# Optimization experiments

Hardware: AMD Instinct MI355X
Metric: run time of the kernel (lower is better)

Reference implementation:

```python
import jax, jax.numpy as jnp
import numpy as np

N = 50000      # nodes
E = 400000     # edges (avg degree 8)
N_IN = 256     # n_in_chan
N_HID = 256    # n_hid_chan


def gcn_conv(x, src, dst, W, b, n):
    """PyG GCNConv: D^{-1/2}(A+I)D^{-1/2} X W^T + b (add_self_loops=True, unit weights)."""
    h = x @ W.T                                           # [n, out]
    # degree over A + I: each node has a self loop (the initial ones) plus in-edges
    deg = jnp.ones((n,), h.dtype).at[dst].add(1.0)        # [n]
    dinv = jax.lax.rsqrt(deg)                             # deg >= 1 always
    norm = dinv[src] * dinv[dst]                          # [E]
    agg = jnp.zeros_like(h).at[dst].add(h[src] * norm[:, None])
    agg = agg + h * (dinv * dinv)[:, None]                # self-loop term, norm = dinv_i^2
    return agg + b


def setup_inputs() -> dict:
    key = jax.random.key(0)
    k1, k2, k3, k4 = jax.random.split(key, 4)
    x = jax.random.normal(k1, (N, N_IN + N_HID), dtype=jnp.float32)
    edge_index = jax.random.randint(k2, (2, E), 0, N, dtype=jnp.int64)
    s1 = 1.0 / np.sqrt(N_IN + N_HID)
    s2 = 1.0 / np.sqrt(N_HID)
    W1 = jax.random.normal(k3, (N_HID, N_IN + N_HID), dtype=jnp.float32) * s1
    W2 = jax.random.normal(k4, (N_HID, N_HID), dtype=jnp.float32) * s2
    b1 = jnp.zeros((N_HID,), jnp.float32)
    b2 = jnp.zeros((N_HID,), jnp.float32)
    return {"x": x, "edge_index": edge_index, "W1": W1, "b1": b1, "W2": W2, "b2": b2}


def reference(x, edge_index, W1, b1, W2, b2):
    src, dst = edge_index[0], edge_index[1]
    h = jax.nn.relu(gcn_conv(x, src, dst, W1, b1, N))
    return gcn_conv(h, src, dst, W2, b2, N)
```

## Files before the change

kernel.cpp:

```cpp
#include <hip/hip_runtime.h>
#include <hip/hip_bf16.h>

#define NN 50000
#define CH 256
#define SLOTS 96
#define G1K 512
#define G2K 256

typedef unsigned short u16;
typedef unsigned int   u32;

using short8 = __attribute__((ext_vector_type(8))) short;
using u16x8  = __attribute__((ext_vector_type(8))) unsigned short;
using f32x4  = __attribute__((ext_vector_type(4))) float;

static __device__ __forceinline__ float4 ld4(const float* p){ return *(const float4*)p; }

static __device__ __forceinline__ u16 f2b(float f){
  u32 u = __float_as_uint(f);
  u = (u + 0x7fffu + ((u >> 16) & 1u)) >> 16;
  return (u16)u;
}
static __device__ __forceinline__ float b2f(u16 b){
  return __uint_as_float(((u32)b) << 16);
}
static __device__ __forceinline__ int pkbf(float lo, float hi){
  __hip_bfloat162 h = __float22bfloat162_rn(make_float2(lo, hi));
  int r; __builtin_memcpy(&r, &h, 4); return r;
}

static __device__ __forceinline__ void gload_lds16(const u16* g, u16* l){
  __builtin_amdgcn_global_load_lds((const __attribute__((address_space(1))) void*)g,
                                   (__attribute__((address_space(3))) void*)l, 16, 0, 0);
}

#define WBAR(vm) do{ \
    asm volatile("s_waitcnt vmcnt(" #vm ") lgkmcnt(0)" ::: "memory"); \
    __builtin_amdgcn_s_barrier(); \
  }while(0)


__global__ void ell_build_kernel(const int* __restrict__ src, const int* __restrict__ dst,
                                 int* __restrict__ deg, int* __restrict__ ell, int E,
                                 const float* __restrict__ X,  u16* __restrict__ Xbf,  int xn4,
                                 const float* __restrict__ W1, u16* __restrict__ W1bf, int w1n4,
                                 const float* __restrict__ W2, u16* __restrict__ W2bf, int w2n4){
  int T = gridDim.x * 256;
  int g = blockIdx.x*256 + threadIdx.x;
  if (g < E){
    int d = dst[g];
    int pos = atomicAdd(&deg[d], 1);
    if (pos < SLOTS) ell[(size_t)d*SLOTS + pos] = src[g];
  }
  for (int i = g; i < xn4; i += T){
    float4 v = ld4(X + (size_t)i*4);
    int2 o = { pkbf(v.x,v.y), pkbf(v.z,v.w) };
    *(int2*)(Xbf + (size_t)i*4) = o;
  }
  for (int i = g; i < w1n4; i += T){
    float4 v = ld4(W1 + (size_t)i*4);
    int2 o = { pkbf(v.x,v.y), pkbf(v.z,v.w) };
    *(int2*)(W1bf + (size_t)i*4) = o;
  }
  for (int i = g; i < w2n4; i += T){
    float4 v = ld4(W2 + (size_t)i*4);
    int2 o = { pkbf(v.x,v.y), pkbf(v.z,v.w) };
    *(int2*)(W2bf + (size_t)i*4) = o;
  }
}


#define G1_GLB(kt, bb) do{ \
    gload_lds16(gA + (size_t)(kt)*32,          &As[bb][wave*512]); \
    gload_lds16(gB + (size_t)(kt)*32,          &Bs[bb][wave*2048]); \
    gload_lds16(gB + (size_t)(kt)*32 + 16*G1K, &Bs[bb][wave*2048 + 512]); \
    gload_lds16(gB + (size_t)(kt)*32 + 32*G1K, &Bs[bb][wave*2048 + 1024]); \
    gload_lds16(gB + (size_t)(kt)*32 + 48*G1K, &Bs[bb][wave*2048 + 1536]); \
  }while(0)

#define G1_COMP(rb) do{ \
    short8 af[4], bq[4]; \
    _Pragma("unroll") \
    for (int i=0;i<4;i++) af[i] = *(const short8*)&As[rb][(i*16 + lm)*32 + lk]; \
    _Pragma("unroll") \
    for (int j=0;j<4;j++) bq[j] = *(const short8*)&Bs[rb][(wave*64 + j*16 + lm)*32 + lk]; \
    _Pragma("unroll") \
    for (int i=0;i<4;i++) \
      _Pragma("unroll") \
      for (int j=0;j<4;j++) \
        acc[i][j] = __builtin_amdgcn_mfma_f32_16x16x32_bf16(af[i], bq[j], acc[i][j], 0, 0, 0); \
  }while(0)

__global__ __launch_bounds__(256, 4) void gemm1_kernel(const u16* __restrict__ A,
                                                       const u16* __restrict__ Bbf,
                                                       u16* __restrict__ C, int M){
  __shared__ u16 As[3][64*32];
  __shared__ u16 Bs[3][256*32];
  int tid = threadIdx.x;
  int wave = tid >> 6, lane = tid & 63;
  int bm = blockIdx.x;

  int ar = bm*64 + wave*16 + (lane>>2); if (ar > M-1) ar = M-1;
  const u16* gA = A + (size_t)ar*G1K + (lane&3)*8;
  const u16* gB = Bbf + (size_t)(wave*64 + (lane>>2))*G1K + (lane&3)*8;

  int lm = lane & 15;
  int lk = (lane >> 4) * 8;

  f32x4 acc[4][4] = {};

  G1_GLB(0, 0);
  G1_GLB(1, 1);
  WBAR(5);

  G1_GLB( 2,2); G1_COMP(0); WBAR(5);
  G1_GLB( 3,0); G1_COMP(1); WBAR(5);
  G1_GLB( 4,1); G1_COMP(2); WBAR(5);
  G1_GLB( 5,2); G1_COMP(0); WBAR(5);
  G1_GLB( 6,0); G1_COMP(1); WBAR(5);
  G1_GLB( 7,1); G1_COMP(2); WBAR(5);
  G1_GLB( 8,2); G1_COMP(0); WBAR(5);
  G1_GLB( 9,0); G1_COMP(1); WBAR(5);
  G1_GLB(10,1); G1_COMP(2); WBAR(5);
  G1_GLB(11,2); G1_COMP(0); WBAR(5);
  G1_GLB(12,0); G1_COMP(1); WBAR(5);
  G1_GLB(13,1); G1_COMP(2); WBAR(5);
  G1_GLB(14,2); G1_COMP(0); WBAR(5);
  G1_GLB(15,0); G1_COMP(1); WBAR(5);
                G1_COMP(2); WBAR(0);
                G1_COMP(0);

  int rb = (lane >> 4) * 4;
  #pragma unroll
  for (int i=0;i<4;i++){
    #pragma unroll
    for (int r=0;r<4;r++){
      int row = bm*64 + i*16 + rb + r;
      if (row < M){
        #pragma unroll
        for (int j=0;j<4;j++){
          int col = wave*64 + j*16 + lm;
          C[(size_t)row*CH + col] = f2b(acc[i][j][r]);
        }
      }
    }
  }
}


#define G2_GLB(kt, bb) do{ \
    gload_lds16(gA + (size_t)(kt)*32,          &As2[bb][wave*512]); \
    gload_lds16(gB + (size_t)(kt)*32,          &Bs2[bb][wave*2048]); \
    gload_lds16(gB + (size_t)(kt)*32 + 16*G2K, &Bs2[bb][wave*2048 + 512]); \
    gload_lds16(gB + (size_t)(kt)*32 + 32*G2K, &Bs2[bb][wave*2048 + 1024]); \
    gload_lds16(gB + (size_t)(kt)*32 + 48*G2K, &Bs2[bb][wave*2048 + 1536]); \
  }while(0)

#define G2_COMP(rb) do{ \
    short8 af[4], bq[4]; \
    _Pragma("unroll") \
    for (int i=0;i<4;i++) af[i] = *(const short8*)&As2[rb][(i*16 + lm)*32 + lk]; \
    _Pragma("unroll") \
    for (int j=0;j<4;j++) bq[j] = *(const short8*)&Bs2[rb][(wave*64 + j*16 + lm)*32 + lk]; \
    _Pragma("unroll") \
    for (int i=0;i<4;i++) \
      _Pragma("unroll") \
      for (int j=0;j<4;j++) \
        acc[i][j] = __builtin_amdgcn_mfma_f32_16x16x32_bf16(af[i], bq[j], acc[i][j], 0, 0, 0); \
  }while(0)

__global__ __launch_bounds__(256, 4) void gemm2_kernel(const u16* __restrict__ A,
                                                       const u16* __restrict__ B,
                                                       float* __restrict__ Cout,
                                                       const float* __restrict__ bias, int M){
  __shared__ u16 As2[3][64*32];
  __shared__ u16 Bs2[3][256*32];
  int tid = threadIdx.x;
  int wave = tid >> 6, lane = tid & 63;
  int bm = blockIdx.x;

  int ar = bm*64 + wave*16 + (lane>>2); if (ar > M-1) ar = M-1;
  const u16* gA = A + (size_t)ar*G2K + (lane&3)*8;
  const u16* gB = B + (size_t)(wave*64 + (lane>>2))*G2K + (lane&3)*8;

  int lm = lane & 15;
  int lk = (lane >> 4) * 8;

  f32x4 acc[4][4] = {};

  G2_GLB(0, 0);
  G2_GLB(1, 1);
  WBAR(5);

  G2_GLB(2,2); G2_COMP(0); WBAR(5);
  G2_GLB(3,0); G2_COMP(1); WBAR(5);
  G2_GLB(4,1); G2_COMP(2); WBAR(5);
  G2_GLB(5,2); G2_COMP(0); WBAR(5);
  G2_GLB(6,0); G2_COMP(1); WBAR(5);
  G2_GLB(7,1); G2_COMP(2); WBAR(5);
               G2_COMP(0); WBAR(0);
               G2_COMP(1);

  float bv[4];
  #pragma unroll
  for (int j=0;j<4;j++) bv[j] = bias[wave*64 + j*16 + lm];

  int rb = (lane >> 4) * 4;
  #pragma unroll
  for (int i=0;i<4;i++){
    #pragma unroll
    for (int r=0;r<4;r++){
      int row = bm*64 + i*16 + rb + r;
      if (row < M){
        #pragma unroll
        for (int j=0;j<4;j++){
          int col = wave*64 + j*16 + lm;
          Cout[(size_t)row*CH + col] = acc[i][j][r] + bv[j];
        }
      }
    }
  }
}


template<bool RELU, bool BIAS, bool OUTBF>
__global__ __launch_bounds__(256) void aggregate_kernel(const u16* __restrict__ h,
                                                        const float* __restrict__ bias,
                                                        const int* __restrict__ deg,
                                                        const int* __restrict__ ell,
                                                        void* __restrict__ outv, int n){
  int wave = threadIdx.x >> 6;
  int lane = threadIdx.x & 63;
  int i = blockIdx.x*4 + wave;
  if (i >= n) return;
  int half = lane >> 5;
  int c = (lane & 31) * 8;

  int degi = deg[i];
  float di = rsqrtf(1.0f + (float)degi);
  int m = degi < SLOTS ? degi : SLOTS;
  const int* row = ell + (size_t)i*SLOTS;

  float acc[8];
  #pragma unroll
  for (int k=0;k<8;k++) acc[k] = 0.f;

  int e = half;
  for (; e + 6 < m; e += 8){
    int s0 = row[e],   s1 = row[e+2], s2 = row[e+4], s3 = row[e+6];
    float n0 = rsqrtf(1.0f + (float)deg[s0]) * di;
    float n1 = rsqrtf(1.0f + (float)deg[s1]) * di;
    float n2 = rsqrtf(1.0f + (float)deg[s2]) * di;
    float n3 = rsqrtf(1.0f + (float)deg[s3]) * di;
    u16x8 h0 = *(const u16x8*)(h + (size_t)s0*CH + c);
    u16x8 h1 = *(const u16x8*)(h + (size_t)s1*CH + c);
    u16x8 h2 = *(const u16x8*)(h + (size_t)s2*CH + c);
    u16x8 h3 = *(const u16x8*)(h + (size_t)s3*CH + c);
    #pragma unroll
    for (int k=0;k<8;k++) acc[k] += b2f(h0[k])*n0;
    #pragma unroll
    for (int k=0;k<8;k++) acc[k] += b2f(h1[k])*n1;
    #pragma unroll
    for (int k=0;k<8;k++) acc[k] += b2f(h2[k])*n2;
    #pragma unroll
    for (int k=0;k<8;k++) acc[k] += b2f(h3[k])*n3;
  }
  for (; e < m; e += 2){
    int s0 = row[e];
    float n0 = rsqrtf(1.0f + (float)deg[s0]) * di;
    u16x8 h0 = *(const u16x8*)(h + (size_t)s0*CH + c);
    #pragma unroll
    for (int k=0;k<8;k++) acc[k] += b2f(h0[k])*n0;
  }

  if (half == 0){
    float w = di*di;
    u16x8 hv = *(const u16x8*)(h + (size_t)i*CH + c);
    #pragma unroll
    for (int k=0;k<8;k++) acc[k] += b2f(hv[k])*w;
    if (BIAS){
      float4 b0 = ld4(bias + c), b1 = ld4(bias + c + 4);
      acc[0] += b0.x; acc[1] += b0.y; acc[2] += b0.z; acc[3] += b0.w;
      acc[4] += b1.x; acc[5] += b1.y; acc[6] += b1.z; acc[7] += b1.w;
    }
  }

  #pragma unroll
  for (int k=0;k<8;k++) acc[k] += __shfl_xor(acc[k], 32, 64);

  if (half == 0){
    if (RELU){
      #pragma unroll
      for (int k=0;k<8;k++) acc[k] = fmaxf(acc[k], 0.f);
    }
    if (OUTBF){
      u16x8 o;
      #pragma unroll
      for (int k=0;k<8;k++) o[k] = f2b(acc[k]);
      *(u16x8*)((u16*)outv + (size_t)i*CH + c) = o;
    } else {
      float* op = (float*)outv + (size_t)i*CH + c;
      *(float4*)op       = make_float4(acc[0],acc[1],acc[2],acc[3]);
      *(float4*)(op + 4) = make_float4(acc[4],acc[5],acc[6],acc[7]);
    }
  }
}


extern "C" void kernel_launch(void* const* d_in, const int* in_sizes, int n_in,
                              void* d_out, int out_size, void* d_ws, size_t ws_size,
                              hipStream_t stream){
  const float* x  = (const float*)d_in[0];
  const int*   ei = (const int*)d_in[1];
  const float* W1 = (const float*)d_in[2];
  const float* b1 = (const float*)d_in[3];
  const float* W2 = (const float*)d_in[4];
  const float* b2 = (const float*)d_in[5];
  float* out = (float*)d_out;

  const int n = NN;
  const int E = in_sizes[1] / 2;
  const int* src = ei;
  const int* dst = ei + E;

  char* ws = (char*)d_ws;
  size_t off = 0;
  auto alloc = [&](size_t bytes)->char* {
    char* p = ws + off;
    off += (bytes + 255) & ~(size_t)255;
    return p;
  };
  u16*   xbf    = (u16*)  alloc((size_t)n*G1K*sizeof(u16));
  u16*   h1bf   = (u16*)  alloc((size_t)n*CH*sizeof(u16));
  u16*   h2bf   = (u16*)  alloc((size_t)n*CH*sizeof(u16));
  u16*   W1bf   = (u16*)  alloc((size_t)CH*G1K*sizeof(u16));
  u16*   W2bf   = (u16*)  alloc((size_t)CH*CH*sizeof(u16));
  int*   deg    = (int*)  alloc((size_t)n*sizeof(int));
  int*   ell    = (int*)  alloc((size_t)n*SLOTS*sizeof(int));
  (void)ws_size;

  u16* g1out = (u16*)d_out;

  hipMemsetAsync(deg, 0, (size_t)n*sizeof(int), stream);
  ell_build_kernel<<<(E+255)/256, 256, 0, stream>>>(src, dst, deg, ell, E,
                                                    x,  xbf,  n*G1K/4,
                                                    W1, W1bf, CH*G1K/4,
                                                    W2, W2bf, CH*CH/4);

  dim3 gg((n+63)/64);

  gemm1_kernel<<<gg, 256, 0, stream>>>(xbf, W1bf, g1out, n);
  aggregate_kernel<true, true, true><<<(n+3)/4, 256, 0, stream>>>(g1out, b1, deg, ell, h1bf, n);

  aggregate_kernel<false, false, true><<<(n+3)/4, 256, 0, stream>>>(h1bf, b2, deg, ell, h2bf, n);
  gemm2_kernel<<<gg, 256, 0, stream>>>(h2bf, W2bf, out, b2, n);
}
```

Before: 333.6 us.

## Fuse fp32-to-bf16 conversion of X into GEMM1 and precompute dinv

Removes the separate pass that converts X (50000x512 fp32) to bf16. GEMM1 now streams fp32 A tiles into LDS with an XOR swizzle and packs them to bf16 in registers before the MFMA. The pipeline is reworked to triple-buffer A and double-buffer B, and occupancy drops to 2 blocks per SM because the fp32 tiles use more LDS. A small kernel also precomputes dinv once, so aggregation loads it instead of computing rsqrt per edge. The trade is one fewer full write and reread of the bf16 copy of X against extra conversion work inside GEMM1 and lower occupancy.

```diff
diff --git a/kernel.cpp b/kernel.cpp
--- a/kernel.cpp
+++ b/kernel.cpp
@@ -29,7 +29,7 @@
   int r; __builtin_memcpy(&r, &h, 4); return r;
 }
 
-static __device__ __forceinline__ void gload_lds16(const u16* g, u16* l){
+static __device__ __forceinline__ void gload_lds16(const void* g, void* l){
   __builtin_amdgcn_global_load_lds((const __attribute__((address_space(1))) void*)g,
                                    (__attribute__((address_space(3))) void*)l, 16, 0, 0);
 }
@@ -42,7 +42,6 @@
 
 __global__ void ell_build_kernel(const int* __restrict__ src, const int* __restrict__ dst,
                                  int* __restrict__ deg, int* __restrict__ ell, int E,
-                                 const float* __restrict__ X,  u16* __restrict__ Xbf,  int xn4,
                                  const float* __restrict__ W1, u16* __restrict__ W1bf, int w1n4,
                                  const float* __restrict__ W2, u16* __restrict__ W2bf, int w2n4){
   int T = gridDim.x * 256;
@@ -52,11 +51,6 @@
     int pos = atomicAdd(&deg[d], 1);
     if (pos < SLOTS) ell[(size_t)d*SLOTS + pos] = src[g];
   }
-  for (int i = g; i < xn4; i += T){
-    float4 v = ld4(X + (size_t)i*4);
-    int2 o = { pkbf(v.x,v.y), pkbf(v.z,v.w) };
-    *(int2*)(Xbf + (size_t)i*4) = o;
-  }
   for (int i = g; i < w1n4; i += T){
     float4 v = ld4(W1 + (size_t)i*4);
     int2 o = { pkbf(v.x,v.y), pkbf(v.z,v.w) };
@@ -69,19 +63,34 @@
   }
 }
 
-
-#define G1_GLB(kt, bb) do{ \
-    gload_lds16(gA + (size_t)(kt)*32,          &As[bb][wave*512]); \
+__global__ void dinv_kernel(const int* __restrict__ deg, float* __restrict__ dinv, int n){
+  int i = blockIdx.x*256 + threadIdx.x;
+  if (i < n) dinv[i] = rsqrtf(1.0f + (float)deg[i]);
+}
+
+
+#define G1_GLB_B(kt, bb) do{ \
     gload_lds16(gB + (size_t)(kt)*32,          &Bs[bb][wave*2048]); \
     gload_lds16(gB + (size_t)(kt)*32 + 16*G1K, &Bs[bb][wave*2048 + 512]); \
     gload_lds16(gB + (size_t)(kt)*32 + 32*G1K, &Bs[bb][wave*2048 + 1024]); \
     gload_lds16(gB + (size_t)(kt)*32 + 48*G1K, &Bs[bb][wave*2048 + 1536]); \
   }while(0)
 
-#define G1_COMP(rb) do{ \
+#define G1_GLB_A(kt, ab) do{ \
+    gload_lds16(gA0 + (size_t)(kt)*32, &Asf[ab][wave*512]); \
+    gload_lds16(gA1 + (size_t)(kt)*32, &Asf[ab][wave*512 + 256]); \
+  }while(0)
+
+#define G1_COMP(ra, rb) do{ \
     short8 af[4], bq[4]; \
     _Pragma("unroll") \
-    for (int i=0;i<4;i++) af[i] = *(const short8*)&As[rb][(i*16 + lm)*32 + lk]; \
+    for (int i=0;i<4;i++){ \
+      int r = i*16 + lm; \
+      float4 f0 = *(const float4*)&Asf[ra][r*32 + ((s0 ^ (lm&7))<<2)]; \
+      float4 f1 = *(const float4*)&Asf[ra][r*32 + ((s1 ^ (lm&7))<<2)]; \
+      int4 p = { pkbf(f0.x,f0.y), pkbf(f0.z,f0.w), pkbf(f1.x,f1.y), pkbf(f1.z,f1.w) }; \
+      af[i] = *(short8*)&p; \
+    } \
     _Pragma("unroll") \
     for (int j=0;j<4;j++) bq[j] = *(const short8*)&Bs[rb][(wave*64 + j*16 + lm)*32 + lk]; \
     _Pragma("unroll") \
@@ -91,44 +100,50 @@
         acc[i][j] = __builtin_amdgcn_mfma_f32_16x16x32_bf16(af[i], bq[j], acc[i][j], 0, 0, 0); \
   }while(0)
 
-__global__ __launch_bounds__(256, 4) void gemm1_kernel(const u16* __restrict__ A,
+__global__ __launch_bounds__(256, 2) void gemm1_kernel(const float* __restrict__ A,
                                                        const u16* __restrict__ Bbf,
                                                        u16* __restrict__ C, int M){
-  __shared__ u16 As[3][64*32];
-  __shared__ u16 Bs[3][256*32];
+  __shared__ float Asf[3][64*32];
+  __shared__ u16   Bs[2][256*32];
   int tid = threadIdx.x;
   int wave = tid >> 6, lane = tid & 63;
   int bm = blockIdx.x;
 
-  int ar = bm*64 + wave*16 + (lane>>2); if (ar > M-1) ar = M-1;
-  const u16* gA = A + (size_t)ar*G1K + (lane&3)*8;
+  int cslot = (lane & 7) ^ (lane >> 3);
+  int r0 = bm*64 + wave*16 + (lane>>3);     if (r0 > M-1) r0 = M-1;
+  int r1 = r0 + 8;                          if (r1 > M-1) r1 = M-1;
+  const float* gA0 = A + (size_t)r0*G1K + cslot*4;
+  const float* gA1 = A + (size_t)r1*G1K + cslot*4;
   const u16* gB = Bbf + (size_t)(wave*64 + (lane>>2))*G1K + (lane&3)*8;
 
   int lm = lane & 15;
   int lk = (lane >> 4) * 8;
+  int s0 = (lane >> 4) * 2;
+  int s1 = s0 + 1;
 
   f32x4 acc[4][4] = {};
 
-  G1_GLB(0, 0);
-  G1_GLB(1, 1);
-  WBAR(5);
-
-  G1_GLB( 2,2); G1_COMP(0); WBAR(5);
-  G1_GLB( 3,0); G1_COMP(1); WBAR(5);
-  G1_GLB( 4,1); G1_COMP(2); WBAR(5);
-  G1_GLB( 5,2); G1_COMP(0); WBAR(5);
-  G1_GLB( 6,0); G1_COMP(1); WBAR(5);
-  G1_GLB( 7,1); G1_COMP(2); WBAR(5);
-  G1_GLB( 8,2); G1_COMP(0); WBAR(5);
-  G1_GLB( 9,0); G1_COMP(1); WBAR(5);
-  G1_GLB(10,1); G1_COMP(2); WBAR(5);
-  G1_GLB(11,2); G1_COMP(0); WBAR(5);
-  G1_GLB(12,0); G1_COMP(1); WBAR(5);
-  G1_GLB(13,1); G1_COMP(2); WBAR(5);
-  G1_GLB(14,2); G1_COMP(0); WBAR(5);
-  G1_GLB(15,0); G1_COMP(1); WBAR(5);
-                G1_COMP(2); WBAR(0);
-                G1_COMP(0);
+  G1_GLB_B(0, 0);
+  G1_GLB_A(0, 0);
+  G1_GLB_A(1, 1);
+  WBAR(2);
+
+  G1_GLB_B( 1,1); G1_COMP(0,0); G1_GLB_A( 2,2); WBAR(2);
+  G1_GLB_B( 2,0); G1_COMP(1,1); G1_GLB_A( 3,0); WBAR(2);
+  G1_GLB_B( 3,1); G1_COMP(2,0); G1_GLB_A( 4,1); WBAR(2);
+  G1_GLB_B( 4,0); G1_COMP(0,1); G1_GLB_A( 5,2); WBAR(2);
+  G1_GLB_B( 5,1); G1_COMP(1,0); G1_GLB_A( 6,0); WBAR(2);
+  G1_GLB_B( 6,0); G1_COMP(2,1); G1_GLB_A( 7,1); WBAR(2);
+  G1_GLB_B( 7,1); G1_COMP(0,0); G1_GLB_A( 8,2); WBAR(2);
+  G1_GLB_B( 8,0); G1_COMP(1,1); G1_GLB_A( 9,0); WBAR(2);
+  G1_GLB_B( 9,1); G1_COMP(2,0); G1_GLB_A(10,1); WBAR(2);
+  G1_GLB_B(10,0); G1_COMP(0,1); G1_GLB_A(11,2); WBAR(2);
+  G1_GLB_B(11,1); G1_COMP(1,0); G1_GLB_A(12,0); WBAR(2);
+  G1_GLB_B(12,0); G1_COMP(2,1); G1_GLB_A(13,1); WBAR(2);
+  G1_GLB_B(13,1); G1_COMP(0,0); G1_GLB_A(14,2); WBAR(2);
+  G1_GLB_B(14,0); G1_COMP(1,1); G1_GLB_A(15,0); WBAR(2);
+  G1_GLB_B(15,1); G1_COMP(2,0);                 WBAR(0);
+                  G1_COMP(0,1);
 
   int rb = (lane >> 4) * 4;
   #pragma unroll
@@ -227,6 +242,7 @@
 __global__ __launch_bounds__(256) void aggregate_kernel(const u16* __restrict__ h,
                                                         const float* __restrict__ bias,
                                                         const int* __restrict__ deg,
+                                                        const float* __restrict__ dinv,
                                                         const int* __restrict__ ell,
                                                         void* __restrict__ outv, int n){
   int wave = threadIdx.x >> 6;
@@ -237,7 +253,7 @@
   int c = (lane & 31) * 8;
 
   int degi = deg[i];
-  float di = rsqrtf(1.0f + (float)degi);
+  float di = dinv[i];
   int m = degi < SLOTS ? degi : SLOTS;
   const int* row = ell + (size_t)i*SLOTS;
 
@@ -248,10 +264,10 @@
   int e = half;
   for (; e + 6 < m; e += 8){
     int s0 = row[e],   s1 = row[e+2], s2 = row[e+4], s3 = row[e+6];
-    float n0 = rsqrtf(1.0f + (float)deg[s0]) * di;
-    float n1 = rsqrtf(1.0f + (float)deg[s1]) * di;
-    float n2 = rsqrtf(1.0f + (float)deg[s2]) * di;
-    float n3 = rsqrtf(1.0f + (float)deg[s3]) * di;
+    float n0 = dinv[s0] * di;
+    float n1 = dinv[s1] * di;
+    float n2 = dinv[s2] * di;
+    float n3 = dinv[s3] * di;
     u16x8 h0 = *(const u16x8*)(h + (size_t)s0*CH + c);
     u16x8 h1 = *(const u16x8*)(h + (size_t)s1*CH + c);
     u16x8 h2 = *(const u16x8*)(h + (size_t)s2*CH + c);
@@ -267,7 +283,7 @@
   }
   for (; e < m; e += 2){
     int s0 = row[e];
-    float n0 = rsqrtf(1.0f + (float)deg[s0]) * di;
+    float n0 = dinv[s0] * di;
     u16x8 h0 = *(const u16x8*)(h + (size_t)s0*CH + c);
     #pragma unroll
     for (int k=0;k<8;k++) acc[k] += b2f(h0[k])*n0;
@@ -330,12 +346,12 @@
     off += (bytes + 255) & ~(size_t)255;
     return p;
   };
-  u16*   xbf    = (u16*)  alloc((size_t)n*G1K*sizeof(u16));
   u16*   h1bf   = (u16*)  alloc((size_t)n*CH*sizeof(u16));
   u16*   h2bf   = (u16*)  alloc((size_t)n*CH*sizeof(u16));
   u16*   W1bf   = (u16*)  alloc((size_t)CH*G1K*sizeof(u16));
   u16*   W2bf   = (u16*)  alloc((size_t)CH*CH*sizeof(u16));
   int*   deg    = (int*)  alloc((size_t)n*sizeof(int));
+  float* dinv   = (float*)alloc((size_t)n*sizeof(float));
   int*   ell    = (int*)  alloc((size_t)n*SLOTS*sizeof(int));
   (void)ws_size;
 
@@ -343,15 +359,15 @@
 
   hipMemsetAsync(deg, 0, (size_t)n*sizeof(int), stream);
   ell_build_kernel<<<(E+255)/256, 256, 0, stream>>>(src, dst, deg, ell, E,
-                                                    x,  xbf,  n*G1K/4,
                                                     W1, W1bf, CH*G1K/4,
                                                     W2, W2bf, CH*CH/4);
+  dinv_kernel<<<(n+255)/256, 256, 0, stream>>>(deg, dinv, n);
 
   dim3 gg((n+63)/64);
 
-  gemm1_kernel<<<gg, 256, 0, stream>>>(xbf, W1bf, g1out, n);
-  aggregate_kernel<true, true, true><<<(n+3)/4, 256, 0, stream>>>(g1out, b1, deg, ell, h1bf, n);
-
-  aggregate_kernel<false, false, true><<<(n+3)/4, 256, 0, stream>>>(h1bf, b2, deg, ell, h2bf, n);
+  gemm1_kernel<<<gg, 256, 0, stream>>>(x, W1bf, g1out, n);
+  aggregate_kernel<true, true, true><<<(n+3)/4, 256, 0, stream>>>(g1out, b1, deg, dinv, ell, h1bf, n);
+
+  aggregate_kernel<false, false, true><<<(n+3)/4, 256, 0, stream>>>(h1bf, b2, deg, dinv, ell, h2bf, n);
   gemm2_kernel<<<gg, 256, 0, stream>>>(h2bf, W2bf, out, b2, n);
 }
```

Measured after the change: 320.7 us. 1.04x faster.
